# Optimization experiments

Measured on AMD Instinct MI355X. Metric: run time of the kernel, lower is better.

## Reference

```python
import jax, jax.numpy as jnp
import numpy as np

NEG_INF = -1.0e9  # matches torch masked_fill value (unused: no mask)

def setup_inputs() -> dict:
    key = jax.random.key(0)
    kq, kk, kv = jax.random.split(key, 3)
    B, Sq, Sk, D = 8, 2048, 2048, 512
    return {
        "query": jax.random.normal(kq, (B, Sq, D), dtype=jnp.float32),
        "key": jax.random.normal(kk, (B, Sk, D), dtype=jnp.float32),
        "value": jax.random.normal(kv, (B, Sk, D), dtype=jnp.float32),
        "temperature": jnp.ones((), dtype=jnp.float32),
    }

def reference(query, key, value, temperature):
    # Squared Euclidean distance via GEMM identity: ||q||^2 + ||k||^2 - 2 q.k
    # (same math as the broadcast sum((q-k)^2, -1), but without [B,Sq,Sk,D] tensor)
    q_sq = jnp.sum(query * query, axis=-1, keepdims=True)          # [B,Sq,1]
    k_sq = jnp.sum(key * key, axis=-1)[:, None, :]                 # [B,1,Sk]
    qk = jnp.einsum("bqd,bkd->bqk", query, key)                    # [B,Sq,Sk]
    distance_squared = q_sq + k_sq - 2.0 * qk
    similarity = -distance_squared / temperature
    attention_weights = jax.nn.softmax(similarity, axis=-1)        # [B,Sq,Sk]
    attended_values = jnp.einsum("bqk,bkd->bqd", attention_weights, value)
    return attended_values, attention_weights
```

## Files before the change

kernel.cpp:

```cpp
#include <hip/hip_runtime.h>

typedef __bf16 bf16_t;
typedef __bf16 bf16x8 __attribute__((ext_vector_type(8)));
typedef __bf16 bf16x4 __attribute__((ext_vector_type(4)));
typedef __bf16 bf16x2 __attribute__((ext_vector_type(2)));
typedef float f32x4 __attribute__((ext_vector_type(4)));

#define NB 8
#define SQ 2048
#define SK 2048
#define DD 512

#define BM 128
#define BN 128
#define BK 32
#define LDK 40

__global__ __launch_bounds__(256, 2) void logits_kernel(
    const float* __restrict__ Q, const float* __restrict__ K,
    const float* __restrict__ tempP, float* __restrict__ logits) {
  __shared__ bf16_t qh[BM][LDK], ql[BM][LDK], kh[BN][LDK], kl[BN][LDK];
  __shared__ float ksred[BN][8];
  const int b = blockIdx.z;
  const int m0 = blockIdx.y * BM;
  const int n0 = blockIdx.x * BN;
  const int tid = threadIdx.x;
  const int lane = tid & 63;
  const int wave = tid >> 6;
  const int wm = (wave >> 1) * 64;
  const int wn = (wave & 1) * 64;
  const int lrow = lane & 15;
  const int quad = lane >> 4;

  const float* Qb = Q + (size_t)b * SQ * DD;
  const float* Kb = K + (size_t)b * SK * DD;

  const int srow = tid >> 3;
  const int scol = (tid & 7) * 4;

  const float* qbase = Qb + (size_t)(m0 + srow) * DD + scol;
  const float* kbase = Kb + (size_t)(n0 + srow) * DD + scol;

  f32x4 acc[4][4];
#pragma unroll
  for (int i = 0; i < 4; i++)
#pragma unroll
    for (int j = 0; j < 4; j++) acc[i][j] = (f32x4){0.f, 0.f, 0.f, 0.f};

  float kss[4] = {0.f, 0.f, 0.f, 0.f};

  float4 pq[4], pk[4];
#pragma unroll
  for (int i = 0; i < 4; i++) {
    pq[i] = *(const float4*)(qbase + (size_t)i * 32 * DD);
    pk[i] = *(const float4*)(kbase + (size_t)i * 32 * DD);
  }

  for (int k0 = 0; k0 < DD; k0 += BK) {
    __syncthreads();
#pragma unroll
    for (int i = 0; i < 4; i++) {
      const int r = srow + i * 32;
      float4 qv = pq[i], kv = pk[i];
      bf16_t q0 = (bf16_t)qv.x, q1 = (bf16_t)qv.y, q2 = (bf16_t)qv.z, q3 = (bf16_t)qv.w;
      bf16x4 qhv = {q0, q1, q2, q3};
      bf16x4 qlv = {(bf16_t)(qv.x - (float)q0), (bf16_t)(qv.y - (float)q1),
                    (bf16_t)(qv.z - (float)q2), (bf16_t)(qv.w - (float)q3)};
      bf16_t c0 = (bf16_t)kv.x, c1 = (bf16_t)kv.y, c2 = (bf16_t)kv.z, c3 = (bf16_t)kv.w;
      bf16x4 khv = {c0, c1, c2, c3};
      bf16x4 klv = {(bf16_t)(kv.x - (float)c0), (bf16_t)(kv.y - (float)c1),
                    (bf16_t)(kv.z - (float)c2), (bf16_t)(kv.w - (float)c3)};
      *(bf16x4*)&qh[r][scol] = qhv;
      *(bf16x4*)&ql[r][scol] = qlv;
      *(bf16x4*)&kh[r][scol] = khv;
      *(bf16x4*)&kl[r][scol] = klv;
      kss[i] = fmaf(kv.x, kv.x, kss[i]);
      kss[i] = fmaf(kv.y, kv.y, kss[i]);
      kss[i] = fmaf(kv.z, kv.z, kss[i]);
      kss[i] = fmaf(kv.w, kv.w, kss[i]);
    }
    __syncthreads();

    if (k0 + BK < DD) {
#pragma unroll
      for (int i = 0; i < 4; i++) {
        pq[i] = *(const float4*)(qbase + (size_t)i * 32 * DD + (k0 + BK));
        pk[i] = *(const float4*)(kbase + (size_t)i * 32 * DD + (k0 + BK));
      }
    }

    bf16x8 bh[4], bl[4];
#pragma unroll
    for (int ni = 0; ni < 4; ni++) {
      bh[ni] = *(const bf16x8*)&kh[wn + ni * 16 + lrow][quad * 8];
      bl[ni] = *(const bf16x8*)&kl[wn + ni * 16 + lrow][quad * 8];
    }
#pragma unroll
    for (int mi = 0; mi < 4; mi++) {
      bf16x8 ah = *(const bf16x8*)&qh[wm + mi * 16 + lrow][quad * 8];
      bf16x8 al = *(const bf16x8*)&ql[wm + mi * 16 + lrow][quad * 8];
#pragma unroll
      for (int ni = 0; ni < 4; ni++) {
        acc[mi][ni] = __builtin_amdgcn_mfma_f32_16x16x32_bf16(ah, bh[ni], acc[mi][ni], 0, 0, 0);
        acc[mi][ni] = __builtin_amdgcn_mfma_f32_16x16x32_bf16(ah, bl[ni], acc[mi][ni], 0, 0, 0);
        acc[mi][ni] = __builtin_amdgcn_mfma_f32_16x16x32_bf16(al, bh[ni], acc[mi][ni], 0, 0, 0);
      }
    }
  }

#pragma unroll
  for (int i = 0; i < 4; i++) ksred[srow + i * 32][tid & 7] = kss[i];
  __syncthreads();

  const float invT = 1.0f / tempP[0];
  float* Lb = logits + (size_t)b * SQ * SK;
#pragma unroll
  for (int ni = 0; ni < 4; ni++) {
    const int nl = wn + ni * 16 + lrow;
    const int n = n0 + nl;
    const float* kr = ksred[nl];
    const float ks = ((kr[0] + kr[1]) + (kr[2] + kr[3])) +
                     ((kr[4] + kr[5]) + (kr[6] + kr[7]));
#pragma unroll
    for (int mi = 0; mi < 4; mi++) {
      const int mbase = m0 + wm + mi * 16 + quad * 4;
#pragma unroll
      for (int r = 0; r < 4; r++) {
        float s = (2.0f * acc[mi][ni][r] - ks) * invT;
        Lb[(size_t)(mbase + r) * SK + n] = s;
      }
    }
  }
}

__global__ __launch_bounds__(256) void softmax_kernel(float* __restrict__ L) {
  float* p = L + (size_t)blockIdx.x * SK;
  const int tid = threadIdx.x;
  const int wave = tid >> 6, lane = tid & 63;

  float4 a = *(const float4*)(p + tid * 4);
  float4 bv = *(const float4*)(p + 1024 + tid * 4);

  float m = fmaxf(fmaxf(fmaxf(a.x, a.y), fmaxf(a.z, a.w)),
                  fmaxf(fmaxf(bv.x, bv.y), fmaxf(bv.z, bv.w)));
#pragma unroll
  for (int off = 32; off; off >>= 1) m = fmaxf(m, __shfl_xor(m, off));
  __shared__ float redm[4];
  if (lane == 0) redm[wave] = m;
  __syncthreads();
  m = fmaxf(fmaxf(redm[0], redm[1]), fmaxf(redm[2], redm[3]));

  float e[8];
  e[0] = __expf(a.x - m);  e[1] = __expf(a.y - m);
  e[2] = __expf(a.z - m);  e[3] = __expf(a.w - m);
  e[4] = __expf(bv.x - m); e[5] = __expf(bv.y - m);
  e[6] = __expf(bv.z - m); e[7] = __expf(bv.w - m);
  float s = ((e[0] + e[1]) + (e[2] + e[3])) + ((e[4] + e[5]) + (e[6] + e[7]));
#pragma unroll
  for (int off = 32; off; off >>= 1) s += __shfl_xor(s, off);
  __shared__ float reds[4];
  if (lane == 0) reds[wave] = s;
  __syncthreads();
  s = (reds[0] + reds[1]) + (reds[2] + reds[3]);

  const float inv = 1.0f / s;
  float4 oa = {e[0] * inv, e[1] * inv, e[2] * inv, e[3] * inv};
  float4 ob = {e[4] * inv, e[5] * inv, e[6] * inv, e[7] * inv};
  *(float4*)(p + tid * 4) = oa;
  *(float4*)(p + 1024 + tid * 4) = ob;
}

__global__ __launch_bounds__(256, 2) void pv_kernel(const float* __restrict__ W,
                                                    const float* __restrict__ V,
                                                    float* __restrict__ O) {
  __shared__ bf16_t wt[BM][LDK];
  __shared__ bf16_t vt[BN][LDK];
  const int b = blockIdx.z;
  const int m0 = blockIdx.y * BM;
  const int d0 = blockIdx.x * BN;
  const int tid = threadIdx.x;
  const int lane = tid & 63;
  const int wave = tid >> 6;
  const int wm = (wave >> 1) * 64;
  const int wn = (wave & 1) * 64;
  const int lrow = lane & 15;
  const int quad = lane >> 4;

  const float* Wb = W + (size_t)b * SQ * SK;
  const float* Vb = V + (size_t)b * SK * DD;

  const int srow = tid >> 3;
  const int scol = (tid & 7) * 4;
  const int p = tid & 15;
  const int c = tid >> 4;

  const float* wbase = Wb + (size_t)(m0 + srow) * SK + scol;
  const float* vbase = Vb + (size_t)(2 * p) * DD + d0 + 4 * c;

  f32x4 acc[4][4];
#pragma unroll
  for (int i = 0; i < 4; i++)
#pragma unroll
    for (int j = 0; j < 4; j++) acc[i][j] = (f32x4){0.f, 0.f, 0.f, 0.f};

  float4 pw[4];
  float4 v0a, v1a, v0b, v1b;
#pragma unroll
  for (int i = 0; i < 4; i++) pw[i] = *(const float4*)(wbase + (size_t)i * 32 * SK);
  v0a = *(const float4*)(vbase);
  v1a = *(const float4*)(vbase + DD);
  v0b = *(const float4*)(vbase + 64);
  v1b = *(const float4*)(vbase + 64 + DD);

  for (int k0 = 0; k0 < SK; k0 += BK) {
    __syncthreads();
#pragma unroll
    for (int i = 0; i < 4; i++) {
      float4 w = pw[i];
      bf16x4 w4 = {(bf16_t)w.x, (bf16_t)w.y, (bf16_t)w.z, (bf16_t)w.w};
      *(bf16x4*)&wt[srow + i * 32][scol] = w4;
    }
    {
      bf16x2 t0 = {(bf16_t)v0a.x, (bf16_t)v1a.x};
      bf16x2 t1 = {(bf16_t)v0a.y, (bf16_t)v1a.y};
      bf16x2 t2 = {(bf16_t)v0a.z, (bf16_t)v1a.z};
      bf16x2 t3 = {(bf16_t)v0a.w, (bf16_t)v1a.w};
      *(bf16x2*)&vt[4 * c + 0][2 * p] = t0;
      *(bf16x2*)&vt[4 * c + 1][2 * p] = t1;
      *(bf16x2*)&vt[4 * c + 2][2 * p] = t2;
      *(bf16x2*)&vt[4 * c + 3][2 * p] = t3;
      bf16x2 u0 = {(bf16_t)v0b.x, (bf16_t)v1b.x};
      bf16x2 u1 = {(bf16_t)v0b.y, (bf16_t)v1b.y};
      bf16x2 u2 = {(bf16_t)v0b.z, (bf16_t)v1b.z};
      bf16x2 u3 = {(bf16_t)v0b.w, (bf16_t)v1b.w};
      *(bf16x2*)&vt[4 * c + 64 + 0][2 * p] = u0;
      *(bf16x2*)&vt[4 * c + 64 + 1][2 * p] = u1;
      *(bf16x2*)&vt[4 * c + 64 + 2][2 * p] = u2;
      *(bf16x2*)&vt[4 * c + 64 + 3][2 * p] = u3;
    }
    __syncthreads();

    if (k0 + BK < SK) {
#pragma unroll
      for (int i = 0; i < 4; i++)
        pw[i] = *(const float4*)(wbase + (size_t)i * 32 * SK + (k0 + BK));
      const float* vb = vbase + (size_t)(k0 + BK) * DD;
      v0a = *(const float4*)(vb);
      v1a = *(const float4*)(vb + DD);
      v0b = *(const float4*)(vb + 64);
      v1b = *(const float4*)(vb + 64 + DD);
    }

    bf16x8 a[4], bb[4];
#pragma unroll
    for (int mi = 0; mi < 4; mi++)
      a[mi] = *(const bf16x8*)&wt[wm + mi * 16 + lrow][quad * 8];
#pragma unroll
    for (int ni = 0; ni < 4; ni++)
      bb[ni] = *(const bf16x8*)&vt[wn + ni * 16 + lrow][quad * 8];
#pragma unroll
    for (int mi = 0; mi < 4; mi++)
#pragma unroll
      for (int ni = 0; ni < 4; ni++)
        acc[mi][ni] = __builtin_amdgcn_mfma_f32_16x16x32_bf16(a[mi], bb[ni], acc[mi][ni], 0, 0, 0);
  }

  float* Ob = O + (size_t)b * SQ * DD;
#pragma unroll
  for (int ni = 0; ni < 4; ni++) {
    const int d = d0 + wn + ni * 16 + lrow;
#pragma unroll
    for (int mi = 0; mi < 4; mi++) {
      const int mbase = m0 + wm + mi * 16 + quad * 4;
#pragma unroll
      for (int r = 0; r < 4; r++) {
        Ob[(size_t)(mbase + r) * DD + d] = acc[mi][ni][r];
      }
    }
  }
}

extern "C" void kernel_launch(void* const* d_in, const int* in_sizes, int n_in,
                              void* d_out, int out_size, void* d_ws, size_t ws_size,
                              hipStream_t stream) {
  const float* Q = (const float*)d_in[0];
  const float* K = (const float*)d_in[1];
  const float* V = (const float*)d_in[2];
  const float* T = (const float*)d_in[3];

  float* outv = (float*)d_out;
  float* logits = outv + (size_t)NB * SQ * DD;

  logits_kernel<<<dim3(SK / BN, SQ / BM, NB), 256, 0, stream>>>(Q, K, T, logits);
  softmax_kernel<<<NB * SQ, 256, 0, stream>>>(logits);
  pv_kernel<<<dim3(DD / BN, SQ / BM, NB), 256, 0, stream>>>(logits, V, outv);
}
```

Measured before the change: 456.5 us.

## Fuse softmax into logits and PV kernels via per-tile partial max/sum

The logits kernel now computes per-row partial max and exp-sum for each 128-column tile and writes them to workspace. The separate softmax kernel is removed: the PV kernel combines the partials into the row max and normalizer, normalizes each logit tile on load, writes the final weights back, and feeds them to the MFMA. The PV kernel is retiled to 64 rows by the full 512 head dimension with 512 threads, so each weight row is read only once instead of four times. This removes one full read-write pass over the large logits matrix, at the cost of extra exp work, shuffles and a larger shared V tile.

```diff
diff --git a/kernel.cpp b/kernel.cpp
--- a/kernel.cpp
+++ b/kernel.cpp
@@ -15,12 +15,15 @@
 #define BN 128
 #define BK 32
 #define LDK 40
+#define NBLK (SK / BN)
 
 __global__ __launch_bounds__(256, 2) void logits_kernel(
     const float* __restrict__ Q, const float* __restrict__ K,
-    const float* __restrict__ tempP, float* __restrict__ logits) {
+    const float* __restrict__ tempP, float* __restrict__ logits,
+    float* __restrict__ Mpart, float* __restrict__ Spart) {
   __shared__ bf16_t qh[BM][LDK], ql[BM][LDK], kh[BN][LDK], kl[BN][LDK];
   __shared__ float ksred[BN][8];
+  __shared__ float mred[BM][2], sred[BM][2];
   const int b = blockIdx.z;
   const int m0 = blockIdx.y * BM;
   const int n0 = blockIdx.x * BN;
@@ -114,88 +117,108 @@
 
   const float invT = 1.0f / tempP[0];
   float* Lb = logits + (size_t)b * SQ * SK;
+  float ks4[4];
 #pragma unroll
   for (int ni = 0; ni < 4; ni++) {
-    const int nl = wn + ni * 16 + lrow;
-    const int n = n0 + nl;
-    const float* kr = ksred[nl];
-    const float ks = ((kr[0] + kr[1]) + (kr[2] + kr[3])) +
-                     ((kr[4] + kr[5]) + (kr[6] + kr[7]));
-#pragma unroll
-    for (int mi = 0; mi < 4; mi++) {
-      const int mbase = m0 + wm + mi * 16 + quad * 4;
-#pragma unroll
-      for (int r = 0; r < 4; r++) {
-        float s = (2.0f * acc[mi][ni][r] - ks) * invT;
-        Lb[(size_t)(mbase + r) * SK + n] = s;
-      }
-    }
+    const float* kr = ksred[wn + ni * 16 + lrow];
+    ks4[ni] = ((kr[0] + kr[1]) + (kr[2] + kr[3])) +
+              ((kr[4] + kr[5]) + (kr[6] + kr[7]));
+  }
+
+#pragma unroll
+  for (int mi = 0; mi < 4; mi++) {
+#pragma unroll
+    for (int r = 0; r < 4; r++) {
+      const int row = wm + mi * 16 + quad * 4 + r;
+      float sv[4];
+#pragma unroll
+      for (int ni = 0; ni < 4; ni++) {
+        sv[ni] = (2.0f * acc[mi][ni][r] - ks4[ni]) * invT;
+        Lb[(size_t)(m0 + row) * SK + (n0 + wn + ni * 16 + lrow)] = sv[ni];
+      }
+      float rm = fmaxf(fmaxf(sv[0], sv[1]), fmaxf(sv[2], sv[3]));
+      rm = fmaxf(rm, __shfl_xor(rm, 1));
+      rm = fmaxf(rm, __shfl_xor(rm, 2));
+      rm = fmaxf(rm, __shfl_xor(rm, 4));
+      rm = fmaxf(rm, __shfl_xor(rm, 8));
+      float rs = __expf(sv[0] - rm) + __expf(sv[1] - rm) +
+                 __expf(sv[2] - rm) + __expf(sv[3] - rm);
+      rs += __shfl_xor(rs, 1);
+      rs += __shfl_xor(rs, 2);
+      rs += __shfl_xor(rs, 4);
+      rs += __shfl_xor(rs, 8);
+      if (lrow == 0) {
+        mred[row][wave & 1] = rm;
+        sred[row][wave & 1] = rs;
+      }
+    }
+  }
+  __syncthreads();
+  if (tid < BM) {
+    const float ma = mred[tid][0], mb = mred[tid][1];
+    const float M = fmaxf(ma, mb);
+    const float S = sred[tid][0] * __expf(ma - M) + sred[tid][1] * __expf(mb - M);
+    const size_t o = ((size_t)b * NBLK + blockIdx.x) * SQ + (m0 + tid);
+    Mpart[o] = M;
+    Spart[o] = S;
   }
 }
 
-__global__ __launch_bounds__(256) void softmax_kernel(float* __restrict__ L) {
-  float* p = L + (size_t)blockIdx.x * SK;
-  const int tid = threadIdx.x;
-  const int wave = tid >> 6, lane = tid & 63;
-
-  float4 a = *(const float4*)(p + tid * 4);
-  float4 bv = *(const float4*)(p + 1024 + tid * 4);
-
-  float m = fmaxf(fmaxf(fmaxf(a.x, a.y), fmaxf(a.z, a.w)),
-                  fmaxf(fmaxf(bv.x, bv.y), fmaxf(bv.z, bv.w)));
-#pragma unroll
-  for (int off = 32; off; off >>= 1) m = fmaxf(m, __shfl_xor(m, off));
-  __shared__ float redm[4];
-  if (lane == 0) redm[wave] = m;
-  __syncthreads();
-  m = fmaxf(fmaxf(redm[0], redm[1]), fmaxf(redm[2], redm[3]));
-
-  float e[8];
-  e[0] = __expf(a.x - m);  e[1] = __expf(a.y - m);
-  e[2] = __expf(a.z - m);  e[3] = __expf(a.w - m);
-  e[4] = __expf(bv.x - m); e[5] = __expf(bv.y - m);
-  e[6] = __expf(bv.z - m); e[7] = __expf(bv.w - m);
-  float s = ((e[0] + e[1]) + (e[2] + e[3])) + ((e[4] + e[5]) + (e[6] + e[7]));
-#pragma unroll
-  for (int off = 32; off; off >>= 1) s += __shfl_xor(s, off);
-  __shared__ float reds[4];
-  if (lane == 0) reds[wave] = s;
-  __syncthreads();
-  s = (reds[0] + reds[1]) + (reds[2] + reds[3]);
-
-  const float inv = 1.0f / s;
-  float4 oa = {e[0] * inv, e[1] * inv, e[2] * inv, e[3] * inv};
-  float4 ob = {e[4] * inv, e[5] * inv, e[6] * inv, e[7] * inv};
-  *(float4*)(p + tid * 4) = oa;
-  *(float4*)(p + 1024 + tid * 4) = ob;
-}
-
-__global__ __launch_bounds__(256, 2) void pv_kernel(const float* __restrict__ W,
-                                                    const float* __restrict__ V,
-                                                    float* __restrict__ O) {
-  __shared__ bf16_t wt[BM][LDK];
-  __shared__ bf16_t vt[BN][LDK];
-  const int b = blockIdx.z;
-  const int m0 = blockIdx.y * BM;
-  const int d0 = blockIdx.x * BN;
+#define PM 64
+
+__global__ __launch_bounds__(512, 2) void pv_kernel(
+    float* __restrict__ L,
+    const float* __restrict__ V,
+    const float* __restrict__ Mpart, const float* __restrict__ Spart,
+    float* __restrict__ O) {
+  __shared__ bf16_t wt[PM][LDK];
+  __shared__ bf16_t vt[DD][LDK];
+  __shared__ float Msh[PM], Ssh[PM];
+  const int b = blockIdx.y;
+  const int m0 = blockIdx.x * PM;
   const int tid = threadIdx.x;
   const int lane = tid & 63;
   const int wave = tid >> 6;
-  const int wm = (wave >> 1) * 64;
-  const int wn = (wave & 1) * 64;
+  const int wn = wave * 64;
   const int lrow = lane & 15;
   const int quad = lane >> 4;
 
-  const float* Wb = W + (size_t)b * SQ * SK;
+  float* Lb = L + (size_t)b * SQ * SK;
   const float* Vb = V + (size_t)b * SK * DD;
+
+  if (tid < 4 * PM) {
+    const int row = tid >> 2;
+    const int i0 = (tid & 3) * 4;
+    float pm[4], ps[4];
+#pragma unroll
+    for (int j = 0; j < 4; j++) {
+      const size_t o = ((size_t)b * NBLK + (i0 + j)) * SQ + (m0 + row);
+      pm[j] = Mpart[o];
+      ps[j] = Spart[o];
+    }
+    float m = fmaxf(fmaxf(pm[0], pm[1]), fmaxf(pm[2], pm[3]));
+    m = fmaxf(m, __shfl_xor(m, 1));
+    m = fmaxf(m, __shfl_xor(m, 2));
+    float s = ps[0] * __expf(pm[0] - m) + ps[1] * __expf(pm[1] - m) +
+              ps[2] * __expf(pm[2] - m) + ps[3] * __expf(pm[3] - m);
+    s += __shfl_xor(s, 1);
+    s += __shfl_xor(s, 2);
+    if ((tid & 3) == 0) {
+      Msh[row] = m;
+      Ssh[row] = 1.0f / s;
+    }
+  }
+  __syncthreads();
 
   const int srow = tid >> 3;
   const int scol = (tid & 7) * 4;
   const int p = tid & 15;
   const int c = tid >> 4;
 
-  const float* wbase = Wb + (size_t)(m0 + srow) * SK + scol;
-  const float* vbase = Vb + (size_t)(2 * p) * DD + d0 + 4 * c;
+  float* wbase = Lb + (size_t)(m0 + srow) * SK + scol;
+  const float* vbase = Vb + (size_t)(2 * p) * DD + 4 * c;
+  const float Mv = Msh[srow];
+  const float Sv = Ssh[srow];
 
   f32x4 acc[4][4];
 #pragma unroll
@@ -203,75 +226,74 @@
 #pragma unroll
     for (int j = 0; j < 4; j++) acc[i][j] = (f32x4){0.f, 0.f, 0.f, 0.f};
 
-  float4 pw[4];
-  float4 v0a, v1a, v0b, v1b;
-#pragma unroll
-  for (int i = 0; i < 4; i++) pw[i] = *(const float4*)(wbase + (size_t)i * 32 * SK);
-  v0a = *(const float4*)(vbase);
-  v1a = *(const float4*)(vbase + DD);
-  v0b = *(const float4*)(vbase + 64);
-  v1b = *(const float4*)(vbase + 64 + DD);
+  float4 pw;
+  float4 va[4], vb2[4];
+  pw = *(const float4*)(wbase);
+#pragma unroll
+  for (int j = 0; j < 4; j++) {
+    va[j] = *(const float4*)(vbase + 128 * j);
+    vb2[j] = *(const float4*)(vbase + 128 * j + DD);
+  }
 
   for (int k0 = 0; k0 < SK; k0 += BK) {
     __syncthreads();
-#pragma unroll
-    for (int i = 0; i < 4; i++) {
-      float4 w = pw[i];
-      bf16x4 w4 = {(bf16_t)w.x, (bf16_t)w.y, (bf16_t)w.z, (bf16_t)w.w};
-      *(bf16x4*)&wt[srow + i * 32][scol] = w4;
-    }
     {
-      bf16x2 t0 = {(bf16_t)v0a.x, (bf16_t)v1a.x};
-      bf16x2 t1 = {(bf16_t)v0a.y, (bf16_t)v1a.y};
-      bf16x2 t2 = {(bf16_t)v0a.z, (bf16_t)v1a.z};
-      bf16x2 t3 = {(bf16_t)v0a.w, (bf16_t)v1a.w};
-      *(bf16x2*)&vt[4 * c + 0][2 * p] = t0;
-      *(bf16x2*)&vt[4 * c + 1][2 * p] = t1;
-      *(bf16x2*)&vt[4 * c + 2][2 * p] = t2;
-      *(bf16x2*)&vt[4 * c + 3][2 * p] = t3;
-      bf16x2 u0 = {(bf16_t)v0b.x, (bf16_t)v1b.x};
-      bf16x2 u1 = {(bf16_t)v0b.y, (bf16_t)v1b.y};
-      bf16x2 u2 = {(bf16_t)v0b.z, (bf16_t)v1b.z};
-      bf16x2 u3 = {(bf16_t)v0b.w, (bf16_t)v1b.w};
-      *(bf16x2*)&vt[4 * c + 64 + 0][2 * p] = u0;
-      *(bf16x2*)&vt[4 * c + 64 + 1][2 * p] = u1;
-      *(bf16x2*)&vt[4 * c + 64 + 2][2 * p] = u2;
-      *(bf16x2*)&vt[4 * c + 64 + 3][2 * p] = u3;
+      float4 w = pw;
+      const float w0 = __expf(w.x - Mv) * Sv;
+      const float w1 = __expf(w.y - Mv) * Sv;
+      const float w2 = __expf(w.z - Mv) * Sv;
+      const float w3 = __expf(w.w - Mv) * Sv;
+      float4 nw;
+      nw.x = w0; nw.y = w1; nw.z = w2; nw.w = w3;
+      *(float4*)(wbase + k0) = nw;
+      bf16x4 w4 = {(bf16_t)w0, (bf16_t)w1, (bf16_t)w2, (bf16_t)w3};
+      *(bf16x4*)&wt[srow][scol] = w4;
+    }
+#pragma unroll
+    for (int j = 0; j < 4; j++) {
+      const int d0 = 4 * c + 128 * j;
+      float4 a0 = va[j], a1 = vb2[j];
+      bf16x2 t0 = {(bf16_t)a0.x, (bf16_t)a1.x};
+      bf16x2 t1 = {(bf16_t)a0.y, (bf16_t)a1.y};
+      bf16x2 t2 = {(bf16_t)a0.z, (bf16_t)a1.z};
+      bf16x2 t3 = {(bf16_t)a0.w, (bf16_t)a1.w};
+      *(bf16x2*)&vt[d0 + 0][2 * p] = t0;
+      *(bf16x2*)&vt[d0 + 1][2 * p] = t1;
+      *(bf16x2*)&vt[d0 + 2][2 * p] = t2;
+      *(bf16x2*)&vt[d0 + 3][2 * p] = t3;
     }
     __syncthreads();
 
     if (k0 + BK < SK) {
-#pragma unroll
-      for (int i = 0; i < 4; i++)
-        pw[i] = *(const float4*)(wbase + (size_t)i * 32 * SK + (k0 + BK));
-      const float* vb = vbase + (size_t)(k0 + BK) * DD;
-      v0a = *(const float4*)(vb);
-      v1a = *(const float4*)(vb + DD);
-      v0b = *(const float4*)(vb + 64);
-      v1b = *(const float4*)(vb + 64 + DD);
-    }
-
-    bf16x8 a[4], bb[4];
-#pragma unroll
-    for (int mi = 0; mi < 4; mi++)
-      a[mi] = *(const bf16x8*)&wt[wm + mi * 16 + lrow][quad * 8];
+      pw = *(const float4*)(wbase + k0 + BK);
+      const float* vbk = vbase + (size_t)(k0 + BK) * DD;
+#pragma unroll
+      for (int j = 0; j < 4; j++) {
+        va[j] = *(const float4*)(vbk + 128 * j);
+        vb2[j] = *(const float4*)(vbk + 128 * j + DD);
+      }
+    }
+
+    bf16x8 bb[4];
 #pragma unroll
     for (int ni = 0; ni < 4; ni++)
       bb[ni] = *(const bf16x8*)&vt[wn + ni * 16 + lrow][quad * 8];
 #pragma unroll
-    for (int mi = 0; mi < 4; mi++)
+    for (int mi = 0; mi < 4; mi++) {
+      bf16x8 a = *(const bf16x8*)&wt[mi * 16 + lrow][quad * 8];
 #pragma unroll
       for (int ni = 0; ni < 4; ni++)
-        acc[mi][ni] = __builtin_amdgcn_mfma_f32_16x16x32_bf16(a[mi], bb[ni], acc[mi][ni], 0, 0, 0);
+        acc[mi][ni] = __builtin_amdgcn_mfma_f32_16x16x32_bf16(a, bb[ni], acc[mi][ni], 0, 0, 0);
+    }
   }
 
   float* Ob = O + (size_t)b * SQ * DD;
 #pragma unroll
   for (int ni = 0; ni < 4; ni++) {
-    const int d = d0 + wn + ni * 16 + lrow;
+    const int d = wn + ni * 16 + lrow;
 #pragma unroll
     for (int mi = 0; mi < 4; mi++) {
-      const int mbase = m0 + wm + mi * 16 + quad * 4;
+      const int mbase = m0 + mi * 16 + quad * 4;
 #pragma unroll
       for (int r = 0; r < 4; r++) {
         Ob[(size_t)(mbase + r) * DD + d] = acc[mi][ni][r];
@@ -291,7 +313,10 @@
   float* outv = (float*)d_out;
   float* logits = outv + (size_t)NB * SQ * DD;
 
-  logits_kernel<<<dim3(SK / BN, SQ / BM, NB), 256, 0, stream>>>(Q, K, T, logits);
-  softmax_kernel<<<NB * SQ, 256, 0, stream>>>(logits);
-  pv_kernel<<<dim3(DD / BN, SQ / BM, NB), 256, 0, stream>>>(logits, V, outv);
+  float* Mpart = (float*)d_ws;
+  float* Spart = Mpart + (size_t)NB * NBLK * SQ;
+
+  logits_kernel<<<dim3(SK / BN, SQ / BM, NB), 256, 0, stream>>>(Q, K, T, logits,
+                                                                Mpart, Spart);
+  pv_kernel<<<dim3(SQ / PM, NB), 512, 0, stream>>>(logits, V, Mpart, Spart, outv);
 }
```

New measurement: 532.0 us. 1.17x slower.
